# Optimization experiments

Hardware: AMD Instinct MI355X
Metric: run time of the kernel (lower is better)

Reference implementation:

```python
import jax, jax.numpy as jnp
import jax.scipy.linalg as jsl
import numpy as np

B, C_IN, T = 32, 64, 256
Z = 32
HID = [256, 256]
K = 3


def conv1d_same(x, W, b):
    # x: (B, C_in, T), W: (C_out, C_in, K) -> (B, C_out, T)
    y = jax.lax.conv_general_dilated(x, W, window_strides=(1,), padding='SAME',
                                     dimension_numbers=('NCH', 'OIH', 'NCH'))
    return y + b[None, :, None]


def setup_inputs() -> dict:
    key = jax.random.key(0)
    ks = jax.random.split(key, 4)
    scale = lambda fan_in: 1.0 / np.sqrt(fan_in)
    x = jax.random.normal(ks[0], (B, C_IN, T), dtype=jnp.float32)
    W0 = jax.random.normal(ks[1], (HID[0], C_IN, K), dtype=jnp.float32) * scale(C_IN * K)
    b0 = jnp.zeros((HID[0],), jnp.float32)
    W1 = jax.random.normal(ks[2], (HID[1], HID[0], K), dtype=jnp.float32) * scale(HID[0] * K)
    b1 = jnp.zeros((HID[1],), jnp.float32)
    W2 = jax.random.normal(ks[3], (3 * Z, HID[1], K), dtype=jnp.float32) * scale(HID[1] * K)
    b2 = jnp.zeros((3 * Z,), jnp.float32)
    return {"x": x, "W0": W0, "b0": b0, "W1": W1, "b1": b1, "W2": W2, "b2": b2}


def reference(x, W0, b0, W1, b1, W2, b2):
    batch, seq_len = x.shape[0], x.shape[-1]
    h = jax.nn.relu(conv1d_same(x, W0, b0))
    h = jax.nn.relu(conv1d_same(h, W1, b1))
    stats = conv1d_same(h, W2, b2)                       # (B, 3z, T)
    z = stats.shape[1] // 3
    mu = stats[:, :z]                                    # (B, z, T)
    prec = jax.nn.softplus(stats[:, z:])                 # (B, 2z, T), precision_activation
    # torch: reshape (B, 2z, T) -> (B, z, 2T), drop last value -> 2T-1 params per (b, z)
    prec = prec.reshape(batch, z, 2 * seq_len)[..., :-1]
    diag = prec[..., :seq_len]                           # (B, z, T)  diagonal entries
    sup = prec[..., seq_len:]                            # (B, z, T-1) superdiagonal entries
    # build upper-bidiagonal precision P = I + diag + superdiag
    i = jnp.arange(seq_len)
    j = jnp.arange(seq_len - 1)
    P = jnp.zeros((batch, z, seq_len, seq_len), dtype=x.dtype)
    P = P.at[..., i, i].set(diag + 1.0)
    P = P.at[..., j, j + 1].set(sup)
    eye = jnp.broadcast_to(jnp.eye(seq_len, dtype=x.dtype), P.shape)
    # covariance upper-triangular factor: solve P @ U = I (P upper triangular)
    cov_u = jsl.solve_triangular(P, eye, lower=False)
    cov_u = jnp.where(jnp.isfinite(cov_u), cov_u, jnp.zeros_like(cov_u))
    scale_tril = jnp.swapaxes(cov_u, -1, -2)             # lower triangular (B, z, T, T)
    return mu, scale_tril
```

## Files before the change

kernel.cpp:

```cpp
#include <hip/hip_runtime.h>
#include <hip/hip_bf16.h>
#include <math.h>

#define BB 32
#define TT 256
#define ZDIM 32

typedef float vf4 __attribute__((ext_vector_type(4)));
typedef short short8 __attribute__((ext_vector_type(8)));
typedef short short4v __attribute__((ext_vector_type(4)));
typedef float f32x4 __attribute__((ext_vector_type(4)));

__device__ __forceinline__ float softplus_f(float v) {
    return fmaxf(v, 0.0f) + log1pf(expf(-fabsf(v)));
}

__device__ __forceinline__ unsigned short f2bf(float f) {
    __hip_bfloat16 h = __float2bfloat16(f);
    return *reinterpret_cast<unsigned short*>(&h);
}

template<int COUT, int CIN>
__device__ void wconv_one(const float* __restrict__ W, unsigned short* __restrict__ Wb,
                          int tid, int nthreads)
{
    const int n = 3 * COUT * CIN;
    for (int idx = tid; idx < n; idx += nthreads) {
        int ci = idx % CIN;
        int q  = idx / CIN;
        int o  = q % COUT;
        int k  = q / COUT;
        Wb[idx] = f2bf(W[o * (CIN * 3) + ci * 3 + k]);
    }
}

__global__ __launch_bounds__(256)
void wconv_kernel(const float* __restrict__ W0, const float* __restrict__ W1,
                  const float* __restrict__ W2, unsigned short* __restrict__ w0b,
                  unsigned short* __restrict__ w1b, unsigned short* __restrict__ w2b)
{
    const int tid = blockIdx.x * blockDim.x + threadIdx.x;
    const int nth = gridDim.x * blockDim.x;
    wconv_one<256, 64>(W0, w0b, tid, nth);
    wconv_one<256, 256>(W1, w1b, tid, nth);
    wconv_one<96, 256>(W2, w2b, tid, nth);
}

template<int CIN, int COUT, int NW, int TTILE, bool IS_STATS, bool XBF16>
__global__ __launch_bounds__(NW * 64, 6)
void convm(const void* __restrict__ xin, const unsigned short* __restrict__ Wb,
           const float* __restrict__ bias, unsigned short* __restrict__ y,
           float* __restrict__ out_mu, float* __restrict__ dd,
           float* __restrict__ ss)
{
    static_assert(TTILE == 32, "epilogue lane mapping assumes TTILE=32");
    constexpr int NT    = NW * 64;
    constexpr int OB    = NW * 16;
    constexpr int CT    = 64;
    constexpr int NTF   = TTILE / 16;
    constexpr int PVN   = (TTILE + 16) / 8;
    constexpr int XROWS = TTILE + 16;
    constexpr int XPAD  = 72;

    __shared__ __attribute__((aligned(16))) unsigned short xsb[XROWS][XPAD];

    const int b    = blockIdx.x;
    const int o0   = blockIdx.y * OB;
    const int t0   = blockIdx.z * TTILE;
    const int tid  = threadIdx.x;
    const int wv   = tid >> 6;
    const int lane = tid & 63;
    const int l15  = lane & 15;
    const int quad = lane >> 4;

    f32x4 acc[NTF];
    {
        f32x4 bv;
        #pragma unroll
        for (int r = 0; r < 4; ++r) bv[r] = bias[o0 + wv * 16 + quad * 4 + r];
        #pragma unroll
        for (int nt = 0; nt < NTF; ++nt) acc[nt] = bv;
    }

    const unsigned short* wrow = Wb + (size_t)(o0 + wv * 16 + l15) * CIN;

    for (int c0 = 0; c0 < CIN; c0 += CT) {
        if (c0) __syncthreads();
        for (int idx = tid; idx < CT * PVN; idx += NT) {
            int ci = idx / PVN;
            int pv = idx - ci * PVN;
            int t8 = t0 - 8 + pv * 8;
            unsigned short v[8];
            if (t8 >= 0 && t8 < TT) {
                if constexpr (XBF16) {
                    short8 xv = *(const short8*)((const unsigned short*)xin
                                 + (size_t)(b * CIN + c0 + ci) * TT + t8);
                    #pragma unroll
                    for (int j = 0; j < 8; ++j) v[j] = (unsigned short)xv[j];
                } else {
                    const float* xp = (const float*)xin
                                      + (size_t)(b * CIN + c0 + ci) * TT + t8;
                    f32x4 lo = *(const f32x4*)xp;
                    f32x4 hi = *(const f32x4*)(xp + 4);
                    #pragma unroll
                    for (int j = 0; j < 4; ++j) {
                        v[j]     = f2bf(lo[j]);
                        v[4 + j] = f2bf(hi[j]);
                    }
                }
            } else {
                #pragma unroll
                for (int j = 0; j < 8; ++j) v[j] = 0;
            }
            #pragma unroll
            for (int j = 0; j < 8; ++j) xsb[pv * 8 + j][ci] = v[j];
        }
        __syncthreads();

        #pragma unroll
        for (int ks = 0; ks < 3; ++ks) {
            #pragma unroll
            for (int kc = 0; kc < CT; kc += 32) {
                short8 af = *(const short8*)(wrow + (size_t)ks * COUT * CIN
                                             + c0 + kc + quad * 8);
                #pragma unroll
                for (int nt = 0; nt < NTF; ++nt) {
                    short8 bf = *(const short8*)&xsb[nt * 16 + l15 + ks + 7][kc + quad * 8];
                    acc[nt] = __builtin_amdgcn_mfma_f32_16x16x32_bf16(af, bf, acc[nt], 0, 0, 0);
                }
            }
        }
    }

    if constexpr (!IS_STATS) {
        __syncthreads();
        unsigned short* eb = &xsb[0][0];
        const int base = wv * 512;
        #pragma unroll
        for (int nt = 0; nt < NTF; ++nt) {
            #pragma unroll
            for (int r = 0; r < 4; ++r)
                eb[base + (quad * 4 + r) * 32 + nt * 16 + l15] =
                    f2bf(fmaxf(acc[nt][r], 0.f));
        }
        const int lr = lane >> 2;
        const int lc = lane & 3;
        short4v a0 = *(const short4v*)&eb[base + lr * 32 + lc * 8];
        short4v a1 = *(const short4v*)&eb[base + lr * 32 + lc * 8 + 4];
        short8 v0;
        #pragma unroll
        for (int j = 0; j < 4; ++j) {
            v0[j] = a0[j]; v0[4 + j] = a1[j];
        }
        unsigned short* yp = y + (size_t)(b * COUT + o0 + wv * 16 + lr) * TT
                             + t0 + lc * 8;
        *(short8*)yp = v0;
    } else {
        #pragma unroll
        for (int nt = 0; nt < NTF; ++nt) {
            int t = t0 + nt * 16 + l15;
            #pragma unroll
            for (int r = 0; r < 4; ++r) {
                int o = o0 + wv * 16 + quad * 4 + r;
                float val = acc[nt][r];
                if (o < ZDIM) {
                    out_mu[(b * ZDIM + o) * TT + t] = val;
                } else {
                    int oc = o - ZDIM;
                    int z  = oc >> 1;
                    float sp = softplus_f(val);
                    if ((oc & 1) == 0) dd[(b * ZDIM + z) * TT + t] = sp + 1.f;
                    else               ss[(b * ZDIM + z) * TT + t] = sp;
                }
            }
        }
    }
}

__global__ __launch_bounds__(256)
void tril_kernel(const float* __restrict__ dd, const float* __restrict__ ss,
                 float* __restrict__ out)
{
    __shared__ float invd[TT];
    __shared__ float tt[TT];

    const int bz  = blockIdx.x;
    const int tid = threadIdx.x;

    {
        float d  = dd[bz * TT + tid];
        float s  = ss[bz * TT + tid];
        float iv = 1.0f / d;
        invd[tid] = iv;
        tt[tid]   = -s * iv;
    }
    __syncthreads();

    const int r0 = (tid >> 6) * 64;
    const int c0 = (tid & 63) * 4;

    float p0 = 1.f, p1 = 1.f, p2 = 1.f, p3 = 1.f;
    for (int k = 0; k < r0 - 1; ++k) {
        float tm = tt[k];
        p0 = (k >= c0    ) ? p0 * tm : p0;
        p1 = (k >= c0 + 1) ? p1 * tm : p1;
        p2 = (k >= c0 + 2) ? p2 * tm : p2;
        p3 = (k >= c0 + 3) ? p3 * tm : p3;
    }
    p0 = (c0     < r0) ? p0 : 0.f;
    p1 = (c0 + 1 < r0) ? p1 : 0.f;
    p2 = (c0 + 2 < r0) ? p2 : 0.f;
    p3 = (c0 + 3 < r0) ? p3 : 0.f;

    float* orow = out + (size_t)bz * TT * TT + (size_t)r0 * TT + c0;

    #pragma unroll 2
    for (int r = r0; r < r0 + 64; ++r) {
        float tm = (r > 0) ? tt[r - 1] : 0.0f;
        p0 = (r == c0    ) ? 1.0f : p0 * tm;
        p1 = (r == c0 + 1) ? 1.0f : p1 * tm;
        p2 = (r == c0 + 2) ? 1.0f : p2 * tm;
        p3 = (r == c0 + 3) ? 1.0f : p3 * tm;
        float id = invd[r];
        vf4 v;
        v.x = p0 * id; v.y = p1 * id; v.z = p2 * id; v.w = p3 * id;
        v.x = isfinite(v.x) ? v.x : 0.0f;
        v.y = isfinite(v.y) ? v.y : 0.0f;
        v.z = isfinite(v.z) ? v.z : 0.0f;
        v.w = isfinite(v.w) ? v.w : 0.0f;
        __builtin_nontemporal_store(v, (vf4*)orow);
        orow += TT;
    }
}

extern "C" void kernel_launch(void* const* d_in, const int* in_sizes, int n_in,
                              void* d_out, int out_size, void* d_ws, size_t ws_size,
                              hipStream_t stream)
{
    const float* x  = (const float*)d_in[0];
    const float* W0 = (const float*)d_in[1];
    const float* b0 = (const float*)d_in[2];
    const float* W1 = (const float*)d_in[3];
    const float* b1 = (const float*)d_in[4];
    const float* W2 = (const float*)d_in[5];
    const float* b2 = (const float*)d_in[6];

    float* out = (float*)d_out;
    float* mu  = out;
    float* st  = out + BB * ZDIM * TT;

    unsigned short* h0b = (unsigned short*)d_ws;
    unsigned short* h1b = h0b + BB * 256 * TT;
    float* dd  = (float*)(h1b + BB * 256 * TT);
    float* ss  = dd + BB * ZDIM * TT;
    unsigned short* w0b = (unsigned short*)(ss + BB * ZDIM * TT);
    unsigned short* w1b = w0b + 3 * 256 * 64;
    unsigned short* w2b = w1b + 3 * 256 * 256;

    wconv_kernel<<<dim3(256), 256, 0, stream>>>(W0, W1, W2, w0b, w1b, w2b);
    convm<64, 256, 4, 32, false, false><<<dim3(BB, 4, 8), 256, 0, stream>>>(
        x, w0b, b0, h0b, nullptr, nullptr, nullptr);
    convm<256, 256, 4, 32, false, true><<<dim3(BB, 4, 8), 256, 0, stream>>>(
        h0b, w1b, b1, h1b, nullptr, nullptr, nullptr);
    convm<256, 96, 3, 32, true, true><<<dim3(BB, 2, 8), 192, 0, stream>>>(
        h1b, w2b, b2, nullptr, mu, dd, ss);
    tril_kernel<<<dim3(BB * ZDIM), 256, 0, stream>>>(dd, ss, st);
}
```

Baseline: 321.1 us.

## Store activations time-major with zero-padded halo rows and read MFMA operands directly

Intermediate activations are stored as (B, T+2, C) bf16, with zero boundary rows cleared in the weight-conversion kernel. The second and third conv layers then read their MFMA B fragments straight from global memory instead of staging a transposed tile in LDS. This removes the LDS staging, the barriers and the LDS-transposed epilogue. In exchange it relies on cache for the three-tap overlap, issues strided 16-byte global loads per lane, and lowers the occupancy hint to 4.

```diff
diff --git a/kernel.cpp b/kernel.cpp
--- a/kernel.cpp
+++ b/kernel.cpp
@@ -5,6 +5,7 @@
 #define BB 32
 #define TT 256
 #define ZDIM 32
+#define TROWS (TT + 2)
 
 typedef float vf4 __attribute__((ext_vector_type(4)));
 typedef short short8 __attribute__((ext_vector_type(8)));
@@ -37,36 +38,44 @@
 __global__ __launch_bounds__(256)
 void wconv_kernel(const float* __restrict__ W0, const float* __restrict__ W1,
                   const float* __restrict__ W2, unsigned short* __restrict__ w0b,
-                  unsigned short* __restrict__ w1b, unsigned short* __restrict__ w2b)
+                  unsigned short* __restrict__ w1b, unsigned short* __restrict__ w2b,
+                  unsigned short* __restrict__ h0t, unsigned short* __restrict__ h1t)
 {
     const int tid = blockIdx.x * blockDim.x + threadIdx.x;
     const int nth = gridDim.x * blockDim.x;
     wconv_one<256, 64>(W0, w0b, tid, nth);
     wconv_one<256, 256>(W1, w1b, tid, nth);
     wconv_one<96, 256>(W2, w2b, tid, nth);
-}
-
-template<int CIN, int COUT, int NW, int TTILE, bool IS_STATS, bool XBF16>
-__global__ __launch_bounds__(NW * 64, 6)
-void convm(const void* __restrict__ xin, const unsigned short* __restrict__ Wb,
-           const float* __restrict__ bias, unsigned short* __restrict__ y,
-           float* __restrict__ out_mu, float* __restrict__ dd,
-           float* __restrict__ ss)
-{
-    static_assert(TTILE == 32, "epilogue lane mapping assumes TTILE=32");
+    const int ng = BB * 2 * (256 / 4);
+    for (int idx = tid; idx < ng; idx += nth) {
+        int cv = idx % (256 / 4);
+        int q  = idx / (256 / 4);
+        int b  = q >> 1;
+        int hi = q & 1;
+        size_t row = (size_t)(b * TROWS + (hi ? TROWS - 1 : 0)) * 256 + cv * 4;
+        short4v z = {0, 0, 0, 0};
+        *(short4v*)&h0t[row] = z;
+        *(short4v*)&h1t[row] = z;
+    }
+}
+
+template<int CIN, int COUT, int NW>
+__global__ __launch_bounds__(NW * 64, 4)
+void conv_stage(const float* __restrict__ xin, const unsigned short* __restrict__ Wb,
+                const float* __restrict__ bias, unsigned short* __restrict__ yt)
+{
     constexpr int NT    = NW * 64;
     constexpr int OB    = NW * 16;
-    constexpr int CT    = 64;
-    constexpr int NTF   = TTILE / 16;
-    constexpr int PVN   = (TTILE + 16) / 8;
-    constexpr int XROWS = TTILE + 16;
+    constexpr int NTF   = 2;
+    constexpr int PVN   = 6;
+    constexpr int XROWS = 48;
     constexpr int XPAD  = 72;
 
     __shared__ __attribute__((aligned(16))) unsigned short xsb[XROWS][XPAD];
 
     const int b    = blockIdx.x;
     const int o0   = blockIdx.y * OB;
-    const int t0   = blockIdx.z * TTILE;
+    const int t0   = blockIdx.z * 32;
     const int tid  = threadIdx.x;
     const int wv   = tid >> 6;
     const int lane = tid & 63;
@@ -82,50 +91,95 @@
         for (int nt = 0; nt < NTF; ++nt) acc[nt] = bv;
     }
 
-    const unsigned short* wrow = Wb + (size_t)(o0 + wv * 16 + l15) * CIN;
-
-    for (int c0 = 0; c0 < CIN; c0 += CT) {
-        if (c0) __syncthreads();
-        for (int idx = tid; idx < CT * PVN; idx += NT) {
-            int ci = idx / PVN;
-            int pv = idx - ci * PVN;
-            int t8 = t0 - 8 + pv * 8;
-            unsigned short v[8];
-            if (t8 >= 0 && t8 < TT) {
-                if constexpr (XBF16) {
-                    short8 xv = *(const short8*)((const unsigned short*)xin
-                                 + (size_t)(b * CIN + c0 + ci) * TT + t8);
-                    #pragma unroll
-                    for (int j = 0; j < 8; ++j) v[j] = (unsigned short)xv[j];
-                } else {
-                    const float* xp = (const float*)xin
-                                      + (size_t)(b * CIN + c0 + ci) * TT + t8;
-                    f32x4 lo = *(const f32x4*)xp;
-                    f32x4 hi = *(const f32x4*)(xp + 4);
-                    #pragma unroll
-                    for (int j = 0; j < 4; ++j) {
-                        v[j]     = f2bf(lo[j]);
-                        v[4 + j] = f2bf(hi[j]);
-                    }
-                }
-            } else {
-                #pragma unroll
-                for (int j = 0; j < 8; ++j) v[j] = 0;
+    for (int idx = tid; idx < CIN * PVN; idx += NT) {
+        int ci = idx / PVN;
+        int pv = idx - ci * PVN;
+        int t8 = t0 - 8 + pv * 8;
+        unsigned short v[8];
+        if (t8 >= 0 && t8 < TT) {
+            const float* xp = xin + (size_t)(b * CIN + ci) * TT + t8;
+            f32x4 lo = *(const f32x4*)xp;
+            f32x4 hi = *(const f32x4*)(xp + 4);
+            #pragma unroll
+            for (int j = 0; j < 4; ++j) {
+                v[j]     = f2bf(lo[j]);
+                v[4 + j] = f2bf(hi[j]);
             }
-            #pragma unroll
-            for (int j = 0; j < 8; ++j) xsb[pv * 8 + j][ci] = v[j];
-        }
-        __syncthreads();
-
+        } else {
+            #pragma unroll
+            for (int j = 0; j < 8; ++j) v[j] = 0;
+        }
+        #pragma unroll
+        for (int j = 0; j < 8; ++j) xsb[pv * 8 + j][ci] = v[j];
+    }
+    __syncthreads();
+
+    const unsigned short* wrow = Wb + (size_t)(o0 + wv * 16 + l15) * CIN + quad * 8;
+
+    #pragma unroll
+    for (int ks = 0; ks < 3; ++ks) {
+        #pragma unroll
+        for (int kc = 0; kc < CIN; kc += 32) {
+            short8 af = *(const short8*)(wrow + (size_t)ks * COUT * CIN + kc);
+            #pragma unroll
+            for (int nt = 0; nt < NTF; ++nt) {
+                short8 bf = *(const short8*)&xsb[nt * 16 + l15 + ks + 7][kc + quad * 8];
+                acc[nt] = __builtin_amdgcn_mfma_f32_16x16x32_bf16(af, bf, acc[nt], 0, 0, 0);
+            }
+        }
+    }
+
+    #pragma unroll
+    for (int nt = 0; nt < NTF; ++nt) {
+        int t = t0 + nt * 16 + l15;
+        short4v v;
+        #pragma unroll
+        for (int r = 0; r < 4; ++r) v[r] = (short)f2bf(fmaxf(acc[nt][r], 0.f));
+        *(short4v*)&yt[(size_t)(b * TROWS + t + 1) * COUT + o0 + wv * 16 + quad * 4] = v;
+    }
+}
+
+template<int CIN, int COUT, int NW, bool IS_STATS>
+__global__ __launch_bounds__(NW * 64, 4)
+void conv_flat(const unsigned short* __restrict__ xt, const unsigned short* __restrict__ Wb,
+               const float* __restrict__ bias, unsigned short* __restrict__ yt,
+               float* __restrict__ out_mu, float* __restrict__ dd,
+               float* __restrict__ ss)
+{
+    constexpr int OB  = NW * 16;
+    constexpr int NTF = 2;
+
+    const int b    = blockIdx.x;
+    const int o0   = blockIdx.y * OB;
+    const int t0   = blockIdx.z * 32;
+    const int tid  = threadIdx.x;
+    const int wv   = tid >> 6;
+    const int lane = tid & 63;
+    const int l15  = lane & 15;
+    const int quad = lane >> 4;
+
+    f32x4 acc[NTF];
+    {
+        f32x4 bv;
+        #pragma unroll
+        for (int r = 0; r < 4; ++r) bv[r] = bias[o0 + wv * 16 + quad * 4 + r];
+        #pragma unroll
+        for (int nt = 0; nt < NTF; ++nt) acc[nt] = bv;
+    }
+
+    const unsigned short* wrow = Wb + (size_t)(o0 + wv * 16 + l15) * CIN + quad * 8;
+    const unsigned short* xrow = xt + (size_t)(b * TROWS + t0 + l15) * CIN + quad * 8;
+
+    #pragma unroll
+    for (int c0 = 0; c0 < CIN; c0 += 64) {
         #pragma unroll
         for (int ks = 0; ks < 3; ++ks) {
             #pragma unroll
-            for (int kc = 0; kc < CT; kc += 32) {
-                short8 af = *(const short8*)(wrow + (size_t)ks * COUT * CIN
-                                             + c0 + kc + quad * 8);
+            for (int kc = 0; kc < 64; kc += 32) {
+                short8 af = *(const short8*)(wrow + (size_t)ks * COUT * CIN + c0 + kc);
                 #pragma unroll
                 for (int nt = 0; nt < NTF; ++nt) {
-                    short8 bf = *(const short8*)&xsb[nt * 16 + l15 + ks + 7][kc + quad * 8];
+                    short8 bf = *(const short8*)(xrow + (size_t)(nt * 16 + ks) * CIN + c0 + kc);
                     acc[nt] = __builtin_amdgcn_mfma_f32_16x16x32_bf16(af, bf, acc[nt], 0, 0, 0);
                 }
             }
@@ -133,28 +187,14 @@
     }
 
     if constexpr (!IS_STATS) {
-        __syncthreads();
-        unsigned short* eb = &xsb[0][0];
-        const int base = wv * 512;
         #pragma unroll
         for (int nt = 0; nt < NTF; ++nt) {
-            #pragma unroll
-            for (int r = 0; r < 4; ++r)
-                eb[base + (quad * 4 + r) * 32 + nt * 16 + l15] =
-                    f2bf(fmaxf(acc[nt][r], 0.f));
-        }
-        const int lr = lane >> 2;
-        const int lc = lane & 3;
-        short4v a0 = *(const short4v*)&eb[base + lr * 32 + lc * 8];
-        short4v a1 = *(const short4v*)&eb[base + lr * 32 + lc * 8 + 4];
-        short8 v0;
-        #pragma unroll
-        for (int j = 0; j < 4; ++j) {
-            v0[j] = a0[j]; v0[4 + j] = a1[j];
-        }
-        unsigned short* yp = y + (size_t)(b * COUT + o0 + wv * 16 + lr) * TT
-                             + t0 + lc * 8;
-        *(short8*)yp = v0;
+            int t = t0 + nt * 16 + l15;
+            short4v v;
+            #pragma unroll
+            for (int r = 0; r < 4; ++r) v[r] = (short)f2bf(fmaxf(acc[nt][r], 0.f));
+            *(short4v*)&yt[(size_t)(b * TROWS + t + 1) * COUT + o0 + wv * 16 + quad * 4] = v;
+        }
     } else {
         #pragma unroll
         for (int nt = 0; nt < NTF; ++nt) {
@@ -249,20 +289,19 @@
     float* mu  = out;
     float* st  = out + BB * ZDIM * TT;
 
-    unsigned short* h0b = (unsigned short*)d_ws;
-    unsigned short* h1b = h0b + BB * 256 * TT;
-    float* dd  = (float*)(h1b + BB * 256 * TT);
+    unsigned short* h0t = (unsigned short*)d_ws;
+    unsigned short* h1t = h0t + (size_t)BB * TROWS * 256;
+    float* dd  = (float*)(h1t + (size_t)BB * TROWS * 256);
     float* ss  = dd + BB * ZDIM * TT;
     unsigned short* w0b = (unsigned short*)(ss + BB * ZDIM * TT);
     unsigned short* w1b = w0b + 3 * 256 * 64;
     unsigned short* w2b = w1b + 3 * 256 * 256;
 
-    wconv_kernel<<<dim3(256), 256, 0, stream>>>(W0, W1, W2, w0b, w1b, w2b);
-    convm<64, 256, 4, 32, false, false><<<dim3(BB, 4, 8), 256, 0, stream>>>(
-        x, w0b, b0, h0b, nullptr, nullptr, nullptr);
-    convm<256, 256, 4, 32, false, true><<<dim3(BB, 4, 8), 256, 0, stream>>>(
-        h0b, w1b, b1, h1b, nullptr, nullptr, nullptr);
-    convm<256, 96, 3, 32, true, true><<<dim3(BB, 2, 8), 192, 0, stream>>>(
-        h1b, w2b, b2, nullptr, mu, dd, ss);
+    wconv_kernel<<<dim3(256), 256, 0, stream>>>(W0, W1, W2, w0b, w1b, w2b, h0t, h1t);
+    conv_stage<64, 256, 4><<<dim3(BB, 4, 8), 256, 0, stream>>>(x, w0b, b0, h0t);
+    conv_flat<256, 256, 4, false><<<dim3(BB, 4, 8), 256, 0, stream>>>(
+        h0t, w1b, b1, h1t, nullptr, nullptr, nullptr);
+    conv_flat<256, 96, 3, true><<<dim3(BB, 2, 8), 192, 0, stream>>>(
+        h1t, w2b, b2, nullptr, mu, dd, ss);
     tril_kernel<<<dim3(BB * ZDIM), 256, 0, stream>>>(dd, ss, st);
 }
```

New measurement: 347.5 us. 8.2% more time.

## Fuse three conv layers into one kernel with halo recompute in LDS

Applied to the files above, without the earlier changes.

Replaces the three separate conv launches with a single kernel in which each block handles one batch and a 32-step time tile. It computes layer 0 and layer 1 over widened halo regions and keeps the intermediate activations in shared memory instead of writing them to global memory. This removes the global round-trips for h0 and h1 and two kernel launches. In exchange it recomputes the halo, launches only 256 blocks of 512 threads with one block per CU, and each block reads the full weight set.

```diff
diff --git a/kernel.cpp b/kernel.cpp
--- a/kernel.cpp
+++ b/kernel.cpp
@@ -46,125 +46,171 @@
     wconv_one<96, 256>(W2, w2b, tid, nth);
 }
 
-template<int CIN, int COUT, int NW, int TTILE, bool IS_STATS, bool XBF16>
-__global__ __launch_bounds__(NW * 64, 6)
-void convm(const void* __restrict__ xin, const unsigned short* __restrict__ Wb,
-           const float* __restrict__ bias, unsigned short* __restrict__ y,
-           float* __restrict__ out_mu, float* __restrict__ dd,
-           float* __restrict__ ss)
-{
-    static_assert(TTILE == 32, "epilogue lane mapping assumes TTILE=32");
-    constexpr int NT    = NW * 64;
-    constexpr int OB    = NW * 16;
-    constexpr int CT    = 64;
-    constexpr int NTF   = TTILE / 16;
-    constexpr int PVN   = (TTILE + 16) / 8;
-    constexpr int XROWS = TTILE + 16;
-    constexpr int XPAD  = 72;
-
-    __shared__ __attribute__((aligned(16))) unsigned short xsb[XROWS][XPAD];
+__global__ __launch_bounds__(512, 1)
+void fused_conv(const float* __restrict__ x,
+                const unsigned short* __restrict__ w0b,
+                const unsigned short* __restrict__ w1b,
+                const unsigned short* __restrict__ w2b,
+                const float* __restrict__ b0, const float* __restrict__ b1,
+                const float* __restrict__ b2,
+                float* __restrict__ mu, float* __restrict__ dd,
+                float* __restrict__ ss)
+{
+    constexpr int XPAD = 72;
+    constexpr int HPAD = 264;
+
+    __shared__ __attribute__((aligned(16))) unsigned short xsb[64][XPAD];
+    __shared__ __attribute__((aligned(16))) unsigned short h0s[48][HPAD];
+    __shared__ __attribute__((aligned(16))) unsigned short h1s[34][HPAD];
 
     const int b    = blockIdx.x;
-    const int o0   = blockIdx.y * OB;
-    const int t0   = blockIdx.z * TTILE;
+    const int t0   = blockIdx.y * 32;
     const int tid  = threadIdx.x;
     const int wv   = tid >> 6;
     const int lane = tid & 63;
     const int l15  = lane & 15;
     const int quad = lane >> 4;
 
-    f32x4 acc[NTF];
-    {
-        f32x4 bv;
-        #pragma unroll
-        for (int r = 0; r < 4; ++r) bv[r] = bias[o0 + wv * 16 + quad * 4 + r];
-        #pragma unroll
-        for (int nt = 0; nt < NTF; ++nt) acc[nt] = bv;
-    }
-
-    const unsigned short* wrow = Wb + (size_t)(o0 + wv * 16 + l15) * CIN;
-
-    for (int c0 = 0; c0 < CIN; c0 += CT) {
-        if (c0) __syncthreads();
-        for (int idx = tid; idx < CT * PVN; idx += NT) {
-            int ci = idx / PVN;
-            int pv = idx - ci * PVN;
-            int t8 = t0 - 8 + pv * 8;
-            unsigned short v[8];
-            if (t8 >= 0 && t8 < TT) {
-                if constexpr (XBF16) {
-                    short8 xv = *(const short8*)((const unsigned short*)xin
-                                 + (size_t)(b * CIN + c0 + ci) * TT + t8);
+    {
+        const int ci = lane;
+        const int t8 = t0 - 16 + wv * 8;
+        unsigned short v[8];
+        if (t8 >= 0 && t8 < TT) {
+            const float* xp = x + (size_t)(b * 64 + ci) * TT + t8;
+            f32x4 lo = *(const f32x4*)xp;
+            f32x4 hi = *(const f32x4*)(xp + 4);
+            #pragma unroll
+            for (int j = 0; j < 4; ++j) { v[j] = f2bf(lo[j]); v[4 + j] = f2bf(hi[j]); }
+        } else {
+            #pragma unroll
+            for (int j = 0; j < 8; ++j) v[j] = 0;
+        }
+        #pragma unroll
+        for (int j = 0; j < 8; ++j) xsb[wv * 8 + j][ci] = v[j];
+    }
+    __syncthreads();
+
+    {
+        f32x4 a1[2][3];
+        #pragma unroll
+        for (int oi = 0; oi < 2; ++oi) {
+            f32x4 bv;
+            #pragma unroll
+            for (int r = 0; r < 4; ++r) bv[r] = b0[(wv + 8 * oi) * 16 + quad * 4 + r];
+            #pragma unroll
+            for (int nt = 0; nt < 3; ++nt) a1[oi][nt] = bv;
+        }
+        const unsigned short* w0r0 = w0b + (size_t)(wv * 16 + l15) * 64 + quad * 8;
+        const unsigned short* w0r1 = w0b + (size_t)((wv + 8) * 16 + l15) * 64 + quad * 8;
+        #pragma unroll
+        for (int ks = 0; ks < 3; ++ks) {
+            #pragma unroll
+            for (int kc = 0; kc < 64; kc += 32) {
+                short8 af0 = *(const short8*)(w0r0 + (size_t)ks * 256 * 64 + kc);
+                short8 af1 = *(const short8*)(w0r1 + (size_t)ks * 256 * 64 + kc);
+                #pragma unroll
+                for (int nt = 0; nt < 3; ++nt) {
+                    short8 bf = *(const short8*)&xsb[nt * 16 + l15 + ks + 7][kc + quad * 8];
+                    a1[0][nt] = __builtin_amdgcn_mfma_f32_16x16x32_bf16(af0, bf, a1[0][nt], 0, 0, 0);
+                    a1[1][nt] = __builtin_amdgcn_mfma_f32_16x16x32_bf16(af1, bf, a1[1][nt], 0, 0, 0);
+                }
+            }
+        }
+        #pragma unroll
+        for (int oi = 0; oi < 2; ++oi) {
+            #pragma unroll
+            for (int nt = 0; nt < 3; ++nt) {
+                int p = nt * 16 + l15;
+                int t = t0 - 8 + p;
+                bool ok = (t >= 0) && (t < TT);
+                short4v v;
+                #pragma unroll
+                for (int r = 0; r < 4; ++r)
+                    v[r] = ok ? (short)f2bf(fmaxf(a1[oi][nt][r], 0.f)) : (short)0;
+                *(short4v*)&h0s[p][(wv + 8 * oi) * 16 + quad * 4] = v;
+            }
+        }
+    }
+    __syncthreads();
+
+    {
+        f32x4 a2[2][3];
+        #pragma unroll
+        for (int oi = 0; oi < 2; ++oi) {
+            f32x4 bv;
+            #pragma unroll
+            for (int r = 0; r < 4; ++r) bv[r] = b1[(wv + 8 * oi) * 16 + quad * 4 + r];
+            #pragma unroll
+            for (int nt = 0; nt < 3; ++nt) a2[oi][nt] = bv;
+        }
+        const unsigned short* w1r0 = w1b + (size_t)(wv * 16 + l15) * 256 + quad * 8;
+        const unsigned short* w1r1 = w1b + (size_t)((wv + 8) * 16 + l15) * 256 + quad * 8;
+        #pragma unroll
+        for (int c0 = 0; c0 < 256; c0 += 64) {
+            #pragma unroll
+            for (int ks = 0; ks < 3; ++ks) {
+                #pragma unroll
+                for (int kc = 0; kc < 64; kc += 32) {
+                    short8 af0 = *(const short8*)(w1r0 + (size_t)ks * 256 * 256 + c0 + kc);
+                    short8 af1 = *(const short8*)(w1r1 + (size_t)ks * 256 * 256 + c0 + kc);
                     #pragma unroll
-                    for (int j = 0; j < 8; ++j) v[j] = (unsigned short)xv[j];
-                } else {
-                    const float* xp = (const float*)xin
-                                      + (size_t)(b * CIN + c0 + ci) * TT + t8;
-                    f32x4 lo = *(const f32x4*)xp;
-                    f32x4 hi = *(const f32x4*)(xp + 4);
-                    #pragma unroll
-                    for (int j = 0; j < 4; ++j) {
-                        v[j]     = f2bf(lo[j]);
-                        v[4 + j] = f2bf(hi[j]);
+                    for (int nt = 0; nt < 3; ++nt) {
+                        constexpr int F2[3] = {6, 22, 24};
+                        short8 bf = *(const short8*)&h0s[F2[nt] + l15 + ks][c0 + kc + quad * 8];
+                        a2[0][nt] = __builtin_amdgcn_mfma_f32_16x16x32_bf16(af0, bf, a2[0][nt], 0, 0, 0);
+                        a2[1][nt] = __builtin_amdgcn_mfma_f32_16x16x32_bf16(af1, bf, a2[1][nt], 0, 0, 0);
                     }
                 }
-            } else {
-                #pragma unroll
-                for (int j = 0; j < 8; ++j) v[j] = 0;
-            }
-            #pragma unroll
-            for (int j = 0; j < 8; ++j) xsb[pv * 8 + j][ci] = v[j];
-        }
-        __syncthreads();
-
-        #pragma unroll
-        for (int ks = 0; ks < 3; ++ks) {
-            #pragma unroll
-            for (int kc = 0; kc < CT; kc += 32) {
-                short8 af = *(const short8*)(wrow + (size_t)ks * COUT * CIN
-                                             + c0 + kc + quad * 8);
-                #pragma unroll
-                for (int nt = 0; nt < NTF; ++nt) {
-                    short8 bf = *(const short8*)&xsb[nt * 16 + l15 + ks + 7][kc + quad * 8];
-                    acc[nt] = __builtin_amdgcn_mfma_f32_16x16x32_bf16(af, bf, acc[nt], 0, 0, 0);
+            }
+        }
+        #pragma unroll
+        for (int oi = 0; oi < 2; ++oi) {
+            #pragma unroll
+            for (int nt = 0; nt < 3; ++nt) {
+                constexpr int P2[3]  = {0, 16, 18};
+                constexpr int TO2[3] = {-1, 15, 17};
+                int p = P2[nt] + l15;
+                int t = t0 + TO2[nt] + l15;
+                bool ok = (t >= 0) && (t < TT);
+                short4v v;
+                #pragma unroll
+                for (int r = 0; r < 4; ++r)
+                    v[r] = ok ? (short)f2bf(fmaxf(a2[oi][nt][r], 0.f)) : (short)0;
+                *(short4v*)&h1s[p][(wv + 8 * oi) * 16 + quad * 4] = v;
+            }
+        }
+    }
+    __syncthreads();
+
+    {
+        const int nu = (wv < 4) ? 2 : 1;
+        for (int i = 0; i < nu; ++i) {
+            const int u  = wv + 8 * i;
+            const int ot = u % 6;
+            const int nt = u / 6;
+            f32x4 a3;
+            #pragma unroll
+            for (int r = 0; r < 4; ++r) a3[r] = b2[ot * 16 + quad * 4 + r];
+            const unsigned short* w2r = w2b + (size_t)(ot * 16 + l15) * 256 + quad * 8;
+            #pragma unroll
+            for (int c0 = 0; c0 < 256; c0 += 64) {
+                #pragma unroll
+                for (int ks = 0; ks < 3; ++ks) {
+                    #pragma unroll
+                    for (int kc = 0; kc < 64; kc += 32) {
+                        short8 af = *(const short8*)(w2r + (size_t)ks * 96 * 256 + c0 + kc);
+                        short8 bf = *(const short8*)&h1s[nt * 16 + l15 + ks][c0 + kc + quad * 8];
+                        a3 = __builtin_amdgcn_mfma_f32_16x16x32_bf16(af, bf, a3, 0, 0, 0);
+                    }
                 }
             }
-        }
-    }
-
-    if constexpr (!IS_STATS) {
-        __syncthreads();
-        unsigned short* eb = &xsb[0][0];
-        const int base = wv * 512;
-        #pragma unroll
-        for (int nt = 0; nt < NTF; ++nt) {
-            #pragma unroll
-            for (int r = 0; r < 4; ++r)
-                eb[base + (quad * 4 + r) * 32 + nt * 16 + l15] =
-                    f2bf(fmaxf(acc[nt][r], 0.f));
-        }
-        const int lr = lane >> 2;
-        const int lc = lane & 3;
-        short4v a0 = *(const short4v*)&eb[base + lr * 32 + lc * 8];
-        short4v a1 = *(const short4v*)&eb[base + lr * 32 + lc * 8 + 4];
-        short8 v0;
-        #pragma unroll
-        for (int j = 0; j < 4; ++j) {
-            v0[j] = a0[j]; v0[4 + j] = a1[j];
-        }
-        unsigned short* yp = y + (size_t)(b * COUT + o0 + wv * 16 + lr) * TT
-                             + t0 + lc * 8;
-        *(short8*)yp = v0;
-    } else {
-        #pragma unroll
-        for (int nt = 0; nt < NTF; ++nt) {
-            int t = t0 + nt * 16 + l15;
+            const int t = t0 + nt * 16 + l15;
             #pragma unroll
             for (int r = 0; r < 4; ++r) {
-                int o = o0 + wv * 16 + quad * 4 + r;
-                float val = acc[nt][r];
+                int o = ot * 16 + quad * 4 + r;
+                float val = a3[r];
                 if (o < ZDIM) {
-                    out_mu[(b * ZDIM + o) * TT + t] = val;
+                    mu[(b * ZDIM + o) * TT + t] = val;
                 } else {
                     int oc = o - ZDIM;
                     int z  = oc >> 1;
@@ -249,20 +295,14 @@
     float* mu  = out;
     float* st  = out + BB * ZDIM * TT;
 
-    unsigned short* h0b = (unsigned short*)d_ws;
-    unsigned short* h1b = h0b + BB * 256 * TT;
-    float* dd  = (float*)(h1b + BB * 256 * TT);
-    float* ss  = dd + BB * ZDIM * TT;
+    float* dd = (float*)d_ws;
+    float* ss = dd + BB * ZDIM * TT;
     unsigned short* w0b = (unsigned short*)(ss + BB * ZDIM * TT);
     unsigned short* w1b = w0b + 3 * 256 * 64;
     unsigned short* w2b = w1b + 3 * 256 * 256;
 
     wconv_kernel<<<dim3(256), 256, 0, stream>>>(W0, W1, W2, w0b, w1b, w2b);
-    convm<64, 256, 4, 32, false, false><<<dim3(BB, 4, 8), 256, 0, stream>>>(
-        x, w0b, b0, h0b, nullptr, nullptr, nullptr);
-    convm<256, 256, 4, 32, false, true><<<dim3(BB, 4, 8), 256, 0, stream>>>(
-        h0b, w1b, b1, h1b, nullptr, nullptr, nullptr);
-    convm<256, 96, 3, 32, true, true><<<dim3(BB, 2, 8), 192, 0, stream>>>(
-        h1b, w2b, b2, nullptr, mu, dd, ss);
+    fused_conv<<<dim3(BB, 8), 512, 0, stream>>>(
+        x, w0b, w1b, w2b, b0, b1, b2, mu, dd, ss);
     tril_kernel<<<dim3(BB * ZDIM), 256, 0, stream>>>(dd, ss, st);
 }
```

Measured after the change: 311.9 us. 2.9% less time.
